# Kernel optimization log

Hardware: AMD Instinct MI355X
Metric: run time of the kernel (lower is better)

The kernel has to match this reference:

```python
import jax, jax.numpy as jnp
import numpy as np

HID = 4096; H = 128; P = 64; N = 128; G = 8; K = 4; CH = 128
INTER = H * P                      # 8192
CONV_DIM = INTER + 2 * G * N       # 10240
PROJ = INTER + CONV_DIM + H        # 18560
EPS = 1e-5


def segsum(x):
    # stable segment-sum: out[..., i, j] = sum_{j < k <= i} x[..., k]; -inf above diagonal
    T = x.shape[-1]
    xe = jnp.repeat(x[..., None], T, axis=-1)          # [..., i, j] = x[..., i]
    strict = jnp.tril(jnp.ones((T, T), bool), -1)
    s = jnp.cumsum(jnp.where(strict, xe, 0.0), axis=-2)
    keep = jnp.tril(jnp.ones((T, T), bool), 0)
    return jnp.where(keep, s, -jnp.inf)


def setup_inputs() -> dict:
    key = jax.random.key(0)
    ks = jax.random.split(key, 6)
    b, L = 2, 2048
    hidden_states = jax.random.normal(ks[0], (b, L, HID), jnp.float32)
    in_proj_w = jax.random.normal(ks[1], (PROJ, HID), jnp.float32) * (HID ** -0.5)
    conv_w = jax.random.normal(ks[2], (CONV_DIM, 1, K), jnp.float32) * 0.2
    conv_b = jax.random.normal(ks[3], (CONV_DIM,), jnp.float32) * 0.02
    dt_bias = jnp.ones((H,), jnp.float32)
    A_log = jnp.log(jnp.arange(1, H + 1, dtype=jnp.float32))
    D = jnp.ones((H,), jnp.float32)
    norm_weight = jnp.ones((INTER,), jnp.float32)
    out_proj_w = jax.random.normal(ks[4], (HID, INTER), jnp.float32) * (INTER ** -0.5)
    return dict(hidden_states=hidden_states, in_proj_w=in_proj_w, conv_w=conv_w, conv_b=conv_b,
                dt_bias=dt_bias, A_log=A_log, D=D, norm_weight=norm_weight, out_proj_w=out_proj_w)


def _mamba2(hidden_states, in_proj_w, conv_w, conv_b, dt_bias, A_log, D, norm_weight, out_proj_w):
    b, L, _ = hidden_states.shape
    nchunk = L // CH  # seq_len chosen to be a multiple of chunk_size (pad_size = 0)

    # in_proj and split into gate | conv path (x,B,C) | dt
    proj = hidden_states @ in_proj_w.T
    gate, hBC, dt = jnp.split(proj, [INTER, INTER + CONV_DIM], axis=-1)

    # causal depthwise conv1d (padding k-1, truncate) + SiLU
    xp = jnp.pad(hBC.transpose(0, 2, 1), ((0, 0), (0, 0), (K - 1, 0)))
    xc = jax.lax.conv_general_dilated(xp, conv_w, (1,), 'VALID',
                                      feature_group_count=CONV_DIM,
                                      dimension_numbers=('NCW', 'OIW', 'NCW'))
    hBC = jax.nn.silu((xc + conv_b[None, :, None]).transpose(0, 2, 1))
    hs, Bx, Cx = jnp.split(hBC, [INTER, INTER + G * N], axis=-1)

    A = -jnp.exp(A_log)                      # [H]
    dt = jax.nn.softplus(dt + dt_bias)       # time_step_limit = (0, inf) -> clamp is no-op

    hs = hs.reshape(b, L, H, P)
    rep = H // G
    Bm = jnp.tile(Bx.reshape(b, L, G, N), (1, 1, rep, 1))   # matches torch .repeat
    Cm = jnp.tile(Cx.reshape(b, L, G, N), (1, 1, rep, 1))

    D_res = D[None, None, :, None] * hs      # [b,L,H,P]

    # discretize and chunk
    X = (hs * dt[..., None]).reshape(b, nchunk, CH, H, P)
    A_dt = (A[None, None, :] * dt).reshape(b, nchunk, CH, H).transpose(0, 3, 1, 2)  # [b,H,c,l]
    Bc = Bm.reshape(b, nchunk, CH, H, N)
    Cc = Cm.reshape(b, nchunk, CH, H, N)
    A_cs = jnp.cumsum(A_dt, axis=-1)

    # 1. intra-chunk (diagonal blocks)
    Lmat = jnp.exp(segsum(A_dt))                              # [b,H,c,l,s]
    Gm = jnp.einsum('bclhn,bcshn->bclsh', Cc, Bc)
    M = Gm * Lmat.transpose(0, 2, 3, 4, 1)                    # [b,c,l,s,H]
    Y_diag = jnp.einsum('bclsh,bcshp->bclhp', M, X)

    # 2. per-chunk states
    decay_states = jnp.exp(A_cs[..., -1:] - A_cs)             # [b,H,c,l]
    B_decay = Bc * decay_states.transpose(0, 2, 3, 1)[..., None]
    states = jnp.einsum('bclhn,bclhp->bchpn', B_decay, X)     # [b,c,H,P,N]

    # 3. inter-chunk recurrence
    states = jnp.concatenate([jnp.zeros_like(states[:, :1]), states], axis=1)
    A_last = jnp.pad(A_cs[..., -1], ((0, 0), (0, 0), (1, 0)))  # [b,H,c+1]
    decay_chunk = jnp.exp(segsum(A_last)).transpose(0, 3, 2, 1)  # [b,c+1,c+1,H]
    new_states = jnp.einsum('bzjh,bzhpn->bjhpn', decay_chunk, states)
    prev_states = new_states[:, :-1]                           # [b,c,H,P,N]

    # 4. state -> output
    sdo = jnp.exp(A_cs).transpose(0, 2, 3, 1)                  # [b,c,l,H]
    Y_off = jnp.einsum('bclhn,bchpn->bclhp', Cc, prev_states) * sdo[..., None]

    y = (Y_diag + Y_off).reshape(b, L, H, P) + D_res
    scan_out = y.reshape(b, L, INTER)

    # gated group RMSNorm (norm_before_gate=False: gate first, then group-RMS)
    xg = scan_out * jax.nn.silu(gate)
    xr = xg.reshape(b, L, G, INTER // G)
    xr = xr * jax.lax.rsqrt(jnp.mean(xr * xr, axis=-1, keepdims=True) + EPS)
    normed = xr.reshape(b, L, INTER) * norm_weight

    return normed @ out_proj_w.T


def reference(hidden_states, in_proj_w, conv_w, conv_b, dt_bias, A_log, D, norm_weight, out_proj_w):
    return _mamba2(hidden_states, in_proj_w, conv_w, conv_b, dt_bias, A_log, D, norm_weight, out_proj_w)
```

## Files before the change

kernel.cpp:

```cpp
#include <hip/hip_runtime.h>

#define NH 128
#define PD 64
#define NSD 128
#define NG 8
#define CHK 128
#define HIDD 4096
#define INTER_D 8192
#define CONV_D 10240
#define PROJ_D 18560
#define SEQ 2048
#define ROWS 4096
#define NCH 16

typedef __attribute__((ext_vector_type(8))) short bf16x8;
typedef __attribute__((ext_vector_type(4))) float f32x4;

__device__ __forceinline__ unsigned short f2bf(float f) {
  unsigned int u = __float_as_uint(f);
  u += 0x7FFF + ((u >> 16) & 1);
  return (unsigned short)(u >> 16);
}
__device__ __forceinline__ float bf2f(unsigned short s) {
  return __uint_as_float(((unsigned int)s) << 16);
}

__device__ __forceinline__ void gld16(const unsigned short* g, unsigned short* l) {
  __builtin_amdgcn_global_load_lds(
      (__attribute__((address_space(1))) const void*)g,
      (__attribute__((address_space(3))) void*)l, 16, 0, 0);
}

#define BAR() __builtin_amdgcn_s_barrier()
#define SCHED() __builtin_amdgcn_sched_barrier(0)
#define VMCNT(n) asm volatile("s_waitcnt vmcnt(" #n ")" ::: "memory")

__device__ __forceinline__ bf16x8 ldsfrag(const unsigned short* slot, int row, int kslot) {
  int byte = row * 128 + (((kslot ^ (row & 7)) << 4));
  return *(const bf16x8*)((const char*)slot + byte);
}

__global__ __launch_bounds__(256) void cvt_kernel(const float* __restrict__ in,
                                                  unsigned short* __restrict__ out,
                                                  size_t n) {
  size_t i = ((size_t)blockIdx.x * 256 + threadIdx.x) * 4;
  if (i < n) {
    float4 f = *(const float4*)(in + i);
    ushort4 o;
    o.x = f2bf(f.x); o.y = f2bf(f.y); o.z = f2bf(f.z); o.w = f2bf(f.w);
    *(ushort4*)(out + i) = o;
  }
}

template <int OUT_BF16>
__global__ __launch_bounds__(512, 2) void gemm256(const unsigned short* __restrict__ A,
                                                  const unsigned short* __restrict__ B,
                                                  unsigned short* __restrict__ outb,
                                                  float* __restrict__ outf,
                                                  int Nreal, int K) {
  __shared__ unsigned short lds[8][8192];
  int tid = threadIdx.x, l = tid & 63, w = tid >> 6;
  int wm = w >> 2, wn = w & 3;
  int il = l & 15, fog = l >> 4;
  int bid = blockIdx.x;
  int xcd = bid & 7, local = bid >> 3;
  int mt = xcd * 2 + (local & 1), nt = local >> 1;
  const unsigned short* Abase = A + (size_t)mt * 256 * K;
  const unsigned short* Bbase = B + (size_t)nt * 256 * K;
  int NT = K >> 6;

  f32x4 acc[2][2][4][2];
#pragma unroll
  for (int a = 0; a < 2; ++a)
#pragma unroll
    for (int b = 0; b < 2; ++b)
#pragma unroll
      for (int m = 0; m < 4; ++m)
#pragma unroll
        for (int n = 0; n < 2; ++n) acc[a][b][m][n] = (f32x4){0.f, 0.f, 0.f, 0.f};

  auto STG = [&](int tt, int ty) {
    int tc = tt < NT ? tt : NT - 1;
    const unsigned short* g = ((ty & 1) ? Bbase : Abase) + (size_t)((ty >> 1) * 128) * K + tc * 64;
    unsigned short* sp = (unsigned short*)lds[(tt & 1) * 4 + ty];
#pragma unroll
    for (int j = 0; j < 2; ++j) {
      int row = (j * 8 + w) * 8 + (l >> 3);
      int scol = ((l & 7) ^ (row & 7)) * 8;
      gld16(g + (size_t)row * K + scol, sp + (j * 8 + w) * 512);
    }
  };

#define LDA(SLOT)                                          \
  _Pragma("unroll") for (int mi = 0; mi < 4; ++mi)         \
  _Pragma("unroll") for (int kk = 0; kk < 2; ++kk)         \
      av[mi][kk] = ldsfrag(SLOT, wm * 64 + mi * 16 + il, kk * 4 + fog);
#define LDB(QN, SLOT)                                      \
  _Pragma("unroll") for (int ni = 0; ni < 2; ++ni)         \
  _Pragma("unroll") for (int kk = 0; kk < 2; ++kk)         \
      bv[QN][ni][kk] = ldsfrag(SLOT, wn * 32 + ni * 16 + il, kk * 4 + fog);
#define MFMA_PH(QM, QN)                                    \
  _Pragma("unroll") for (int mi = 0; mi < 4; ++mi)         \
  _Pragma("unroll") for (int ni = 0; ni < 2; ++ni)         \
  _Pragma("unroll") for (int kk = 0; kk < 2; ++kk)         \
      acc[QM][QN][mi][ni] = __builtin_amdgcn_mfma_f32_16x16x32_bf16( \
          av[mi][kk], bv[QN][ni][kk], acc[QM][QN][mi][ni], 0, 0, 0);

  STG(0, 0); STG(0, 1); STG(0, 3); STG(0, 2);
  VMCNT(2);
  BAR(); SCHED();

  for (int t = 0; t < NT; ++t) {
    const unsigned short* sA0 = lds[(t & 1) * 4 + 0];
    const unsigned short* sB0 = lds[(t & 1) * 4 + 1];
    const unsigned short* sA1 = lds[(t & 1) * 4 + 2];
    const unsigned short* sB1 = lds[(t & 1) * 4 + 3];
    bf16x8 av[4][2], bv[2][2][2];
    LDA(sA0); LDB(0, sB0); LDB(1, sB1);
    STG(t + 1, 0); STG(t + 1, 1);
    BAR();
    __builtin_amdgcn_s_setprio(1);
    MFMA_PH(0, 0);
    __builtin_amdgcn_s_setprio(0);
    VMCNT(4);
    BAR(); SCHED();
    STG(t + 1, 3);
    __builtin_amdgcn_s_setprio(1);
    MFMA_PH(0, 1);
    __builtin_amdgcn_s_setprio(0);
    BAR();
    LDA(sA1);
    STG(t + 1, 2);
    BAR();
    __builtin_amdgcn_s_setprio(1);
    MFMA_PH(1, 0);
    __builtin_amdgcn_s_setprio(0);
    BAR();
    __builtin_amdgcn_s_setprio(1);
    MFMA_PH(1, 1);
    __builtin_amdgcn_s_setprio(0);
    VMCNT(2);
    BAR(); SCHED();
  }

  int rl = (l >> 4) * 4;
#pragma unroll
  for (int qm = 0; qm < 2; ++qm)
#pragma unroll
    for (int qn = 0; qn < 2; ++qn)
#pragma unroll
      for (int mi = 0; mi < 4; ++mi)
#pragma unroll
        for (int ni = 0; ni < 2; ++ni) {
          int grow = mt * 256 + qm * 128 + wm * 64 + mi * 16 + rl;
          int gcol = nt * 256 + qn * 128 + wn * 32 + ni * 16 + il;
          if (!OUT_BF16 || gcol < Nreal) {
#pragma unroll
            for (int r = 0; r < 4; ++r) {
              float v = acc[qm][qn][mi][ni][r];
              if (OUT_BF16)
                outb[(size_t)(grow + r) * Nreal + gcol] = f2bf(v);
              else
                outf[(size_t)(grow + r) * Nreal + gcol] = v;
            }
          }
        }
#undef LDA
#undef LDB
#undef MFMA_PH
}

__global__ __launch_bounds__(128) void dts_kernel(const unsigned short* __restrict__ proj,
                                                  const float* __restrict__ dt_bias,
                                                  const float* __restrict__ A_log,
                                                  float* __restrict__ dtg,
                                                  float* __restrict__ acsg) {
  int bc = blockIdx.x;
  int h = threadIdx.x;
  int b = bc >> 4, c = bc & 15;
  float A = -__expf(A_log[h]);
  float bias = dt_bias[h];
  float cum = 0.f;
  int row0 = b * SEQ + c * CHK;
  for (int ll = 0; ll < CHK; ++ll) {
    float x = bf2f(proj[(size_t)(row0 + ll) * PROJ_D + (PROJ_D - NH) + h]) + bias;
    float d = (x > 20.f) ? x : log1pf(expf(x));
    dtg[(size_t)(row0 + ll) * NH + h] = d;
    cum += A * d;
    acsg[(((size_t)bc * NH) + h) * CHK + ll] = cum;
  }
}

__global__ __launch_bounds__(256) void conv_kernel(const unsigned short* __restrict__ proj,
                                                   const float* __restrict__ cw,
                                                   const float* __restrict__ cb,
                                                   unsigned short* __restrict__ xbc) {
  int ch = blockIdx.x * 256 + threadIdx.x;
  int row = blockIdx.y;
  int b = row >> 11, ll = row & 2047;
  float acc = cb[ch];
#pragma unroll
  for (int k = 0; k < 4; ++k) {
    int l2 = ll - 3 + k;
    if (l2 >= 0)
      acc += bf2f(proj[(size_t)(b * SEQ + l2) * PROJ_D + INTER_D + ch]) * cw[ch * 4 + k];
  }
  float s = acc / (1.f + __expf(-acc));
  xbc[(size_t)row * CONV_D + ch] = f2bf(s);
}

__global__ __launch_bounds__(256) void e1b_kernel(const unsigned short* __restrict__ xbc,
                                                  const float* __restrict__ dtg,
                                                  const float* __restrict__ acsg,
                                                  float* __restrict__ states) {
  int bid = blockIdx.x;
  int h = bid & 127, c = (bid >> 7) & 15, b = bid >> 11;
  int g = h & 7;
  int row0 = b * SEQ + c * CHK;
  __shared__ __align__(16) char smem[52736];
  unsigned short* XT = (unsigned short*)smem;
  unsigned short* BdT = (unsigned short*)(smem + 17408);
  float* Acs = (float*)(smem + 52224);
  int tid = threadIdx.x, lane = tid & 63, wv = tid >> 6;
  int fo = (lane >> 4) * 8, il = lane & 15, rl = (lane >> 4) * 4;
  if (tid < 128) Acs[tid] = acsg[(((size_t)(b * NCH + c) * NH) + h) * CHK + tid];
  __syncthreads();
#pragma unroll
  for (int j = 0; j < 4; ++j) {
    int q = tid + j * 256;
    int ll = q >> 3, p0 = (q & 7) * 8;
    int row = row0 + ll;
    float dtv = dtg[(size_t)row * NH + h];
    int4 raw = *(const int4*)(xbc + (size_t)row * CONV_D + h * PD + p0);
    unsigned short* u = (unsigned short*)&raw;
#pragma unroll
    for (int e = 0; e < 8; ++e) XT[(p0 + e) * 136 + ll] = f2bf(bf2f(u[e]) * dtv);
  }
#pragma unroll
  for (int j = 0; j < 8; ++j) {
    int q = tid + j * 256;
    int ll = q >> 4, n0 = (q & 15) * 8;
    float dec = __expf(Acs[CHK - 1] - Acs[ll]);
    int4 raw = *(const int4*)(xbc + (size_t)(row0 + ll) * CONV_D + INTER_D + g * NSD + n0);
    unsigned short* u = (unsigned short*)&raw;
#pragma unroll
    for (int e = 0; e < 8; ++e) BdT[(n0 + e) * 136 + ll] = f2bf(bf2f(u[e]) * dec);
  }
  __syncthreads();
  f32x4 st[8];
#pragma unroll
  for (int i = 0; i < 8; ++i) st[i] = (f32x4){0.f, 0.f, 0.f, 0.f};
#pragma unroll
  for (int ks = 0; ks < 4; ++ks) {
    bf16x8 a = *(const bf16x8*)&XT[(wv * 16 + il) * 136 + ks * 32 + fo];
#pragma unroll
    for (int ni = 0; ni < 8; ++ni) {
      bf16x8 bb = *(const bf16x8*)&BdT[(ni * 16 + il) * 136 + ks * 32 + fo];
      st[ni] = __builtin_amdgcn_mfma_f32_16x16x32_bf16(a, bb, st[ni], 0, 0, 0);
    }
  }
  size_t base = ((size_t)(b * NH + h) * NCH + c) * (PD * NSD);
#pragma unroll
  for (int ni = 0; ni < 8; ++ni) {
    int n = ni * 16 + il;
#pragma unroll
    for (int r = 0; r < 4; ++r) {
      int p = wv * 16 + rl + r;
      states[base + p * NSD + n] = st[ni][r];
    }
  }
}

__global__ __launch_bounds__(256) void e2_kernel(const float* __restrict__ acsg,
                                                 float* __restrict__ states) {
  int bid = blockIdx.x;
  int bh = bid >> 2, pg = bid & 3;
  int b = bh >> 7;
  int t = threadIdx.x;
  float S[8];
#pragma unroll
  for (int j = 0; j < 8; ++j) S[j] = 0.f;
  for (int c = 0; c < NCH; ++c) {
    float alast = acsg[(((size_t)((b * NCH + c) * NH) + (bh & 127))) * CHK + (CHK - 1)];
    float dec = __expf(alast);
    size_t base = ((size_t)bh * NCH + c) * (PD * NSD) + (size_t)pg * 2048;
#pragma unroll
    for (int j = 0; j < 8; ++j) {
      size_t e = base + (size_t)j * 256 + t;
      float v = states[e];
      states[e] = S[j];
      S[j] = S[j] * dec + v;
    }
  }
}

__global__ __launch_bounds__(512) void e13_kernel(const unsigned short* __restrict__ xbc,
                                                  const float* __restrict__ dtg,
                                                  const float* __restrict__ acsg,
                                                  const float* __restrict__ states,
                                                  const float* __restrict__ Dp,
                                                  float* __restrict__ yb) {
  int bid = blockIdx.x;
  int h = bid & 127, c = (bid >> 7) & 15, b = bid >> 11;
  int g = h & 7;
  int row0 = b * SEQ + c * CHK;
  __shared__ __align__(16) char smem[70144];
  unsigned short* Cst = (unsigned short*)smem;
  unsigned short* Bst = (unsigned short*)(smem + 10240);
  unsigned short* Mt = (unsigned short*)smem;
  unsigned short* Ct = (unsigned short*)smem;
  unsigned short* XT = (unsigned short*)(smem + 34816);
  unsigned short* Sp = (unsigned short*)(smem + 52224);
  float* Acs = (float*)(smem + 69632);
  int tid = threadIdx.x, lane = tid & 63, wv = tid >> 6;
  int fo = (lane >> 4) * 8, il = lane & 15, rl = (lane >> 4) * 4;
  if (tid < 128) Acs[tid] = acsg[(((size_t)(b * NCH + c) * NH) + h) * CHK + tid];

  f32x4 gm[8];
#pragma unroll
  for (int i = 0; i < 8; ++i) gm[i] = (f32x4){0.f, 0.f, 0.f, 0.f};
  int srow = tid >> 2, scol = (tid & 3) * 8;
  for (int kc = 0; kc < 4; ++kc) {
    __syncthreads();
    *(int4*)(Cst + srow * 40 + scol) =
        *(const int4*)(xbc + (size_t)(row0 + srow) * CONV_D + INTER_D + NG * NSD + g * NSD + kc * 32 + scol);
    *(int4*)(Bst + srow * 40 + scol) =
        *(const int4*)(xbc + (size_t)(row0 + srow) * CONV_D + INTER_D + g * NSD + kc * 32 + scol);
    __syncthreads();
    bf16x8 a = *(const bf16x8*)&Cst[(wv * 16 + il) * 40 + fo];
#pragma unroll
    for (int ni = 0; ni < 8; ++ni) {
      bf16x8 bb = *(const bf16x8*)&Bst[(ni * 16 + il) * 40 + fo];
      gm[ni] = __builtin_amdgcn_mfma_f32_16x16x32_bf16(a, bb, gm[ni], 0, 0, 0);
    }
  }
  __syncthreads();
#pragma unroll
  for (int ni = 0; ni < 8; ++ni) {
    int s = ni * 16 + il;
#pragma unroll
    for (int r = 0; r < 4; ++r) {
      int ll = wv * 16 + rl + r;
      float v = (s <= ll) ? gm[ni][r] * __expf(Acs[ll] - Acs[s]) : 0.f;
      Mt[ll * 136 + s] = f2bf(v);
    }
  }
#pragma unroll
  for (int j = 0; j < 2; ++j) {
    int q = tid + j * 512;
    int ll = q >> 3, p0 = (q & 7) * 8;
    int row = row0 + ll;
    float dtv = dtg[(size_t)row * NH + h];
    int4 raw = *(const int4*)(xbc + (size_t)row * CONV_D + h * PD + p0);
    unsigned short* u = (unsigned short*)&raw;
#pragma unroll
    for (int e = 0; e < 8; ++e) XT[(p0 + e) * 136 + ll] = f2bf(bf2f(u[e]) * dtv);
  }
  size_t sbase = ((size_t)(b * NH + h) * NCH + c) * (PD * NSD);
#pragma unroll
  for (int j = 0; j < 2; ++j) {
    int q = tid + j * 512;
    int p = q >> 4, n0 = (q & 15) * 8;
    unsigned short tmp[8];
#pragma unroll
    for (int e = 0; e < 8; ++e) tmp[e] = f2bf(states[sbase + p * NSD + n0 + e]);
    *(int4*)(Sp + p * 136 + n0) = *(int4*)tmp;
  }
  __syncthreads();
  f32x4 yd[4];
#pragma unroll
  for (int i = 0; i < 4; ++i) yd[i] = (f32x4){0.f, 0.f, 0.f, 0.f};
#pragma unroll
  for (int ks = 0; ks < 4; ++ks) {
    bf16x8 a = *(const bf16x8*)&Mt[(wv * 16 + il) * 136 + ks * 32 + fo];
#pragma unroll
    for (int pi = 0; pi < 4; ++pi) {
      bf16x8 bb = *(const bf16x8*)&XT[(pi * 16 + il) * 136 + ks * 32 + fo];
      yd[pi] = __builtin_amdgcn_mfma_f32_16x16x32_bf16(a, bb, yd[pi], 0, 0, 0);
    }
  }
  __syncthreads();
#pragma unroll
  for (int j = 0; j < 4; ++j) {
    int q = tid + j * 512;
    int ll = q >> 4, n0 = (q & 15) * 8;
    *(int4*)(Ct + ll * 136 + n0) =
        *(const int4*)(xbc + (size_t)(row0 + ll) * CONV_D + INTER_D + NG * NSD + g * NSD + n0);
  }
  __syncthreads();
  f32x4 yo[4];
#pragma unroll
  for (int i = 0; i < 4; ++i) yo[i] = (f32x4){0.f, 0.f, 0.f, 0.f};
#pragma unroll
  for (int ks = 0; ks < 4; ++ks) {
    bf16x8 a = *(const bf16x8*)&Ct[(wv * 16 + il) * 136 + ks * 32 + fo];
#pragma unroll
    for (int pi = 0; pi < 4; ++pi) {
      bf16x8 bb = *(const bf16x8*)&Sp[(pi * 16 + il) * 136 + ks * 32 + fo];
      yo[pi] = __builtin_amdgcn_mfma_f32_16x16x32_bf16(a, bb, yo[pi], 0, 0, 0);
    }
  }
  float dv = Dp[h];
#pragma unroll
  for (int pi = 0; pi < 4; ++pi) {
    int p = pi * 16 + il;
#pragma unroll
    for (int r = 0; r < 4; ++r) {
      int ll = wv * 16 + rl + r;
      int row = row0 + ll;
      float hsv = bf2f(xbc[(size_t)row * CONV_D + h * PD + p]);
      yb[(size_t)row * INTER_D + h * PD + p] =
          yd[pi][r] + yo[pi][r] * __expf(Acs[ll]) + dv * hsv;
    }
  }
}

__global__ __launch_bounds__(256) void fnorm_kernel(const float* __restrict__ yb,
                                                    const unsigned short* __restrict__ proj,
                                                    const float* __restrict__ nw,
                                                    unsigned short* __restrict__ normed) {
  int row = blockIdx.x >> 3;
  int gg = blockIdx.x & 7;
  int t = threadIdx.x;
  float v[4];
  float ss = 0.f;
#pragma unroll
  for (int j = 0; j < 4; ++j) {
    int ch = gg * 1024 + j * 256 + t;
    float val = yb[(size_t)row * INTER_D + ch];
    float gt = bf2f(proj[(size_t)row * PROJ_D + ch]);
    val *= gt / (1.f + __expf(-gt));
    v[j] = val;
    ss += val * val;
  }
  __shared__ float sred[256];
  sred[t] = ss;
  __syncthreads();
  for (int ofs = 128; ofs > 0; ofs >>= 1) {
    if (t < ofs) sred[t] += sred[t + ofs];
    __syncthreads();
  }
  float rms = rsqrtf(sred[0] / 1024.f + 1e-5f);
#pragma unroll
  for (int j = 0; j < 4; ++j) {
    int ch = gg * 1024 + j * 256 + t;
    normed[(size_t)row * INTER_D + ch] = f2bf(v[j] * rms * nw[ch]);
  }
}

extern "C" void kernel_launch(void* const* d_in, const int* in_sizes, int n_in,
                              void* d_out, int out_size, void* d_ws, size_t ws_size,
                              hipStream_t stream) {
  (void)in_sizes; (void)n_in; (void)out_size; (void)ws_size;
  const float* hs = (const float*)d_in[0];
  const float* w1 = (const float*)d_in[1];
  const float* cw = (const float*)d_in[2];
  const float* cb = (const float*)d_in[3];
  const float* dtb = (const float*)d_in[4];
  const float* alog = (const float*)d_in[5];
  const float* Dp = (const float*)d_in[6];
  const float* nw = (const float*)d_in[7];
  const float* w2 = (const float*)d_in[8];
  float* out = (float*)d_out;
  char* ws = (char*)d_ws;

  unsigned short* hsb = (unsigned short*)(ws);
  unsigned short* w1b = (unsigned short*)(ws + 33554432);
  unsigned short* w2b = (unsigned short*)(ws + 186646528);
  unsigned short* proj = (unsigned short*)(ws + 253755392);
  unsigned short* xbc = (unsigned short*)(ws + 405798912);
  float* dtg = (float*)(ws + 489684992);
  float* acsg = (float*)(ws + 491782144);
  float* states = (float*)(ws + 493879296);
  float* yb = (float*)(ws + 628097024);
  unsigned short* normed = (unsigned short*)(ws);

  cvt_kernel<<<dim3(16384), dim3(256), 0, stream>>>(hs, hsb, (size_t)ROWS * HIDD);
  cvt_kernel<<<dim3(74240), dim3(256), 0, stream>>>(w1, w1b, (size_t)PROJ_D * HIDD);
  cvt_kernel<<<dim3(32768), dim3(256), 0, stream>>>(w2, w2b, (size_t)HIDD * INTER_D);

  gemm256<1><<<dim3(16 * 73), dim3(512), 0, stream>>>(hsb, w1b, proj, nullptr,
                                                      PROJ_D, HIDD);
  dts_kernel<<<dim3(32), dim3(128), 0, stream>>>(proj, dtb, alog, dtg, acsg);
  conv_kernel<<<dim3(40, 4096), dim3(256), 0, stream>>>(proj, cw, cb, xbc);
  e1b_kernel<<<dim3(4096), dim3(256), 0, stream>>>(xbc, dtg, acsg, states);
  e2_kernel<<<dim3(1024), dim3(256), 0, stream>>>(acsg, states);
  e13_kernel<<<dim3(4096), dim3(512), 0, stream>>>(xbc, dtg, acsg, states, Dp, yb);
  fnorm_kernel<<<dim3(32768), dim3(256), 0, stream>>>(yb, proj, nw, normed);
  gemm256<0><<<dim3(16 * 16), dim3(512), 0, stream>>>(normed, w2b, nullptr, out,
                                                      HIDD, INTER_D);
}
```

Measured before the change: 1.461 ms.

## Use 128x128-tile GEMM for out_proj to fill more CUs

```diff
diff --git a/kernel.cpp b/kernel.cpp
--- a/kernel.cpp
+++ b/kernel.cpp
@@ -142,6 +142,7 @@
     VMCNT(2);
     BAR(); SCHED();
   }
+  VMCNT(0);
 
   int rl = (l >> 4) * 4;
 #pragma unroll
@@ -170,6 +171,72 @@
 #undef MFMA_PH
 }
 
+__global__ __launch_bounds__(256) void gemm128(const unsigned short* __restrict__ A,
+                                               const unsigned short* __restrict__ B,
+                                               float* __restrict__ outf,
+                                               int N, int K, int nmt) {
+  __shared__ unsigned short As[128 * 64];
+  __shared__ unsigned short Bs[128 * 64];
+  int tid = threadIdx.x, l = tid & 63, w = tid >> 6;
+  int wm = w >> 1, wn = w & 1;
+  int il = l & 15, fog = l >> 4;
+  int bid = blockIdx.x;
+  int cpx = nmt >> 3;
+  int mt = (bid & 7) * cpx + ((bid >> 3) % cpx);
+  int nt = (bid >> 3) / cpx;
+  const unsigned short* Ab = A + (size_t)mt * 128 * K;
+  const unsigned short* Bb = B + (size_t)nt * 128 * K;
+
+  f32x4 acc[4][4];
+#pragma unroll
+  for (int i = 0; i < 4; ++i)
+#pragma unroll
+    for (int j = 0; j < 4; ++j) acc[i][j] = (f32x4){0.f, 0.f, 0.f, 0.f};
+
+  for (int k0 = 0; k0 < K; k0 += 64) {
+    __syncthreads();
+#pragma unroll
+    for (int j = 0; j < 4; ++j) {
+      int row = (j * 4 + w) * 8 + (l >> 3);
+      int scol = ((l & 7) ^ (row & 7)) * 8;
+      gld16(Ab + (size_t)row * K + k0 + scol, As + (j * 4 + w) * 512);
+      gld16(Bb + (size_t)row * K + k0 + scol, Bs + (j * 4 + w) * 512);
+    }
+    __syncthreads();
+    bf16x8 av[4][2], bv[4][2];
+#pragma unroll
+    for (int mi = 0; mi < 4; ++mi)
+#pragma unroll
+      for (int kk = 0; kk < 2; ++kk)
+        av[mi][kk] = ldsfrag(As, wm * 64 + mi * 16 + il, kk * 4 + fog);
+#pragma unroll
+    for (int ni = 0; ni < 4; ++ni)
+#pragma unroll
+      for (int kk = 0; kk < 2; ++kk)
+        bv[ni][kk] = ldsfrag(Bs, wn * 64 + ni * 16 + il, kk * 4 + fog);
+#pragma unroll
+    for (int mi = 0; mi < 4; ++mi)
+#pragma unroll
+      for (int ni = 0; ni < 4; ++ni)
+#pragma unroll
+        for (int kk = 0; kk < 2; ++kk)
+          acc[mi][ni] = __builtin_amdgcn_mfma_f32_16x16x32_bf16(
+              av[mi][kk], bv[ni][kk], acc[mi][ni], 0, 0, 0);
+  }
+
+  int rl = (l >> 4) * 4;
+#pragma unroll
+  for (int mi = 0; mi < 4; ++mi)
+#pragma unroll
+    for (int ni = 0; ni < 4; ++ni) {
+      int grow = mt * 128 + wm * 64 + mi * 16 + rl;
+      int gcol = nt * 128 + wn * 64 + ni * 16 + il;
+#pragma unroll
+      for (int r = 0; r < 4; ++r)
+        outf[(size_t)(grow + r) * N + gcol] = acc[mi][ni][r];
+    }
+}
+
 __global__ __launch_bounds__(128) void dts_kernel(const unsigned short* __restrict__ proj,
                                                   const float* __restrict__ dt_bias,
                                                   const float* __restrict__ A_log,
@@ -182,6 +249,7 @@
   float bias = dt_bias[h];
   float cum = 0.f;
   int row0 = b * SEQ + c * CHK;
+#pragma unroll 4
   for (int ll = 0; ll < CHK; ++ll) {
     float x = bf2f(proj[(size_t)(row0 + ll) * PROJ_D + (PROJ_D - NH) + h]) + bias;
     float d = (x > 20.f) ? x : log1pf(expf(x));
@@ -487,6 +555,5 @@
   e2_kernel<<<dim3(1024), dim3(256), 0, stream>>>(acsg, states);
   e13_kernel<<<dim3(4096), dim3(512), 0, stream>>>(xbc, dtg, acsg, states, Dp, yb);
   fnorm_kernel<<<dim3(32768), dim3(256), 0, stream>>>(yb, proj, nw, normed);
-  gemm256<0><<<dim3(16 * 16), dim3(512), 0, stream>>>(normed, w2b, nullptr, out,
-                                                      HIDD, INTER_D);
-}
+  gemm128<<<dim3(1024), dim3(256), 0, stream>>>(normed, w2b, out, HIDD, INTER_D, 32);
+}
```

Measured after the change: 1.583 ms. 8.4% more time.
